# Performance work log

Measured on AMD Instinct MI355X. Metric: run time of the kernel, lower is better.

Reference implementation:

```python
import jax, jax.numpy as jnp
import numpy as np

N = 8192          # num nodes
F = 256           # feature_size
D = 128           # graph_embedding_size
E = 262144        # num edges (avg degree 32)
SLOPE = 0.2       # cfg.negativeslope
NEG_INF = -9e15   # matches torch's -9000000000000000.0 mask value


def setup_inputs() -> dict:
    key = jax.random.key(0)
    k1, k2, k3, k4 = jax.random.split(key, 4)
    X = jax.random.normal(k1, (N, F), dtype=jnp.float32)
    edge_index = jax.random.randint(k2, (2, E), 0, N, dtype=jnp.int64)
    # glorot init for Ws, xavier_uniform(gain=1.414) for a
    lim_ws = np.sqrt(6.0 / (F + D)).astype(np.float32)
    Ws = jax.random.uniform(k3, (F, D), jnp.float32, -lim_ws, lim_ws)
    lim_a = (1.414 * np.sqrt(6.0 / (2 * D + 1))).astype(np.float32)
    a = jax.random.uniform(k4, (2 * D, 1), jnp.float32, -lim_a, lim_a)
    return {"edge_index": edge_index, "X": X, "Ws": Ws, "a": a}


def reference(edge_index, X, Ws, a):
    # dense adjacency mask from edge list (sparse_coo_tensor(...).to_dense())
    adj = jnp.zeros((N, N), jnp.float32).at[edge_index[0], edge_index[1]].set(1.0)
    Wh = X @ Ws                                   # [N, D]
    # GAT-style score: Wh1_i + Wh2_j, then leaky relu
    e = jax.nn.leaky_relu(Wh @ a[:D] + (Wh @ a[D:]).T, SLOPE)  # [N, N]
    scores = jnp.where(adj > 0, e, NEG_INF)
    att = jax.nn.softmax(scores, axis=1)          # masked row softmax
    return jax.nn.elu(att @ Wh)                   # [N, D]
```

## Files before the change

### kernel.cpp

```cpp
#include <hip/hip_runtime.h>
#include <math.h>

#define N_NODES 8192
#define FDIM 256
#define DDIM 128
#define SLOPE 0.2f
#define ELLW 128

typedef __attribute__((ext_vector_type(8))) short bf16x8;
typedef __attribute__((ext_vector_type(4))) float f32x4;

__device__ __forceinline__ unsigned short f2bf(float f) {
    unsigned u = __float_as_uint(f);
    u += 0x7fffu + ((u >> 16) & 1u);
    return (unsigned short)(u >> 16);
}
__device__ __forceinline__ float bf2f(unsigned short h) {
    return __uint_as_float(((unsigned)h) << 16);
}

__global__ __launch_bounds__(256) void prep_k(const float* __restrict__ Ws,
                                              unsigned short* __restrict__ Wthi,
                                              unsigned short* __restrict__ Wtlo,
                                              unsigned* __restrict__ cnt) {
    int b = blockIdx.x, t = threadIdx.x;
    cnt[b * 256 + t] = 0u;
    if (b >= 8) return;
    __shared__ float ls[32][129];
    int k0 = b * 32;
#pragma unroll
    for (int i = 0; i < 16; i++) {
        int lin = t + 256 * i;
        int kk = lin >> 7, col = lin & 127;
        ls[kk][col] = Ws[(size_t)(k0 + kk) * DDIM + col];
    }
    __syncthreads();
    int col = t >> 1, part = t & 1;
#pragma unroll
    for (int g = 0; g < 4; g++) {
        ushort4 h, l;
        float v0 = ls[part * 16 + g * 4 + 0][col];
        float v1 = ls[part * 16 + g * 4 + 1][col];
        float v2 = ls[part * 16 + g * 4 + 2][col];
        float v3 = ls[part * 16 + g * 4 + 3][col];
        h.x = f2bf(v0); l.x = f2bf(v0 - bf2f(h.x));
        h.y = f2bf(v1); l.y = f2bf(v1 - bf2f(h.y));
        h.z = f2bf(v2); l.z = f2bf(v2 - bf2f(h.z));
        h.w = f2bf(v3); l.w = f2bf(v3 - bf2f(h.w));
        size_t o = (size_t)col * FDIM + k0 + part * 16 + g * 4;
        *(ushort4*)(Wthi + o) = h;
        *(ushort4*)(Wtlo + o) = l;
    }
}

__global__ __launch_bounds__(256) void build_ell(const int* __restrict__ edge, int E,
                                                 unsigned* __restrict__ cnt,
                                                 unsigned* __restrict__ ell) {
    int e = blockIdx.x * blockDim.x + threadIdx.x;
    if (e >= E) return;
    int r = edge[e];
    int c = edge[E + e];
    unsigned slot = atomicAdd(&cnt[r], 1u);
    if (slot < ELLW) ell[(size_t)r * ELLW + slot] = (unsigned)c;
}

__global__ __launch_bounds__(256) void gemm_mfma2(const float* __restrict__ X,
                                                  const unsigned short* __restrict__ Wthi,
                                                  const unsigned short* __restrict__ Wtlo,
                                                  const float* __restrict__ a,
                                                  unsigned short* __restrict__ WhB,
                                                  float* __restrict__ s1,
                                                  float* __restrict__ s2) {
    __shared__ unsigned short Ah[16 * 264], Al[16 * 264];
    __shared__ unsigned short Bh[128 * 72], Bl[128 * 72];
    __shared__ float ps1[64], ps2[64];
    int t = threadIdx.x;
    int w = t >> 6, lane = t & 63, lr = lane & 15, kg = lane >> 4;
    int row0 = blockIdx.x * 16;
    int colbase = w * 32;

    const float4* Xg = (const float4*)(X + (size_t)row0 * FDIM);
#pragma unroll
    for (int i = 0; i < 4; i++) {
        int lin = t + 256 * i;
        int r = lin >> 6, q = lin & 63;
        float4 v = Xg[r * 64 + q];
        ushort4 h, l;
        h.x = f2bf(v.x); l.x = f2bf(v.x - bf2f(h.x));
        h.y = f2bf(v.y); l.y = f2bf(v.y - bf2f(h.y));
        h.z = f2bf(v.z); l.z = f2bf(v.z - bf2f(h.z));
        h.w = f2bf(v.w); l.w = f2bf(v.w - bf2f(h.w));
        *(ushort4*)(Ah + r * 264 + q * 4) = h;
        *(ushort4*)(Al + r * 264 + q * 4) = l;
    }

    f32x4 acc0 = (f32x4){0.f, 0.f, 0.f, 0.f};
    f32x4 acc1 = (f32x4){0.f, 0.f, 0.f, 0.f};

    for (int c = 0; c < 4; c++) {
        if (c) __syncthreads();
#pragma unroll
        for (int i = 0; i < 4; i++) {
            int lin = t + 256 * i;
            int col = lin >> 3, q = lin & 7;
            size_t src = (size_t)col * FDIM + c * 64 + q * 8;
            *(uint4*)(Bh + col * 72 + q * 8) = *(const uint4*)(Wthi + src);
            *(uint4*)(Bl + col * 72 + q * 8) = *(const uint4*)(Wtlo + src);
        }
        __syncthreads();
#pragma unroll
        for (int ks = 0; ks < 2; ks++) {
            int ko = c * 64 + ks * 32;
            bf16x8 ahi = *(bf16x8*)(Ah + lr * 264 + ko + kg * 8);
            bf16x8 alo = *(bf16x8*)(Al + lr * 264 + ko + kg * 8);
            int c0 = colbase + lr, c1 = colbase + 16 + lr;
            bf16x8 bh0 = *(bf16x8*)(Bh + c0 * 72 + ks * 32 + kg * 8);
            bf16x8 bl0 = *(bf16x8*)(Bl + c0 * 72 + ks * 32 + kg * 8);
            bf16x8 bh1 = *(bf16x8*)(Bh + c1 * 72 + ks * 32 + kg * 8);
            bf16x8 bl1 = *(bf16x8*)(Bl + c1 * 72 + ks * 32 + kg * 8);
            acc0 = __builtin_amdgcn_mfma_f32_16x16x32_bf16(ahi, bh0, acc0, 0, 0, 0);
            acc0 = __builtin_amdgcn_mfma_f32_16x16x32_bf16(ahi, bl0, acc0, 0, 0, 0);
            acc0 = __builtin_amdgcn_mfma_f32_16x16x32_bf16(alo, bh0, acc0, 0, 0, 0);
            acc1 = __builtin_amdgcn_mfma_f32_16x16x32_bf16(ahi, bh1, acc1, 0, 0, 0);
            acc1 = __builtin_amdgcn_mfma_f32_16x16x32_bf16(ahi, bl1, acc1, 0, 0, 0);
            acc1 = __builtin_amdgcn_mfma_f32_16x16x32_bf16(alo, bh1, acc1, 0, 0, 0);
        }
    }

#pragma unroll
    for (int r = 0; r < 4; r++) {
        int row = row0 + kg * 4 + r;
        int c0 = colbase + lr, c1 = colbase + 16 + lr;
        float v0 = acc0[r], v1 = acc1[r];
        WhB[(size_t)row * DDIM + c0] = f2bf(v0);
        WhB[(size_t)row * DDIM + c1] = f2bf(v1);
        float q1 = v0 * a[c0] + v1 * a[c1];
        float q2 = v0 * a[DDIM + c0] + v1 * a[DDIM + c1];
        for (int o = 1; o < 16; o <<= 1) {
            q1 += __shfl_xor(q1, o, 16);
            q2 += __shfl_xor(q2, o, 16);
        }
        if (lr == 0) { ps1[w * 16 + kg * 4 + r] = q1; ps2[w * 16 + kg * 4 + r] = q2; }
    }
    __syncthreads();
    if (t < 16) {
        s1[row0 + t] = (ps1[t] + ps1[16 + t]) + (ps1[32 + t] + ps1[48 + t]);
        s2[row0 + t] = (ps2[t] + ps2[16 + t]) + (ps2[32 + t] + ps2[48 + t]);
    }
}

__global__ __launch_bounds__(256) void row_wave_k(const unsigned* __restrict__ cnt,
                                                  const unsigned* __restrict__ ell,
                                                  const float* __restrict__ s1v,
                                                  const float* __restrict__ s2v,
                                                  const unsigned short* __restrict__ WhB,
                                                  float* __restrict__ out) {
    __shared__ unsigned bmw[4][256];
    __shared__ float    pl[4][ELLW];
    __shared__ unsigned jl[4][ELLW];

    int w = threadIdx.x >> 6, lane = threadIdx.x & 63;
    int i = blockIdx.x * 4 + w;
    const ushort2* WhB2 = (const ushort2*)WhB;

    ((uint4*)bmw[w])[lane] = make_uint4(0u, 0u, 0u, 0u);
    unsigned deg = cnt[i];
    if (deg > ELLW) deg = ELLW;
    __syncthreads();

    if (deg == 0u) {
        float sx = 0.f, sy = 0.f;
        for (int rr = 0; rr < N_NODES; rr++) {
            ushort2 u = WhB2[(size_t)rr * 64 + lane];
            sx += bf2f(u.x); sy += bf2f(u.y);
        }
        sx *= (1.0f / N_NODES); sy *= (1.0f / N_NODES);
        sx = sx > 0.f ? sx : __expf(sx) - 1.f;
        sy = sy > 0.f ? sy : __expf(sy) - 1.f;
        ((float2*)out)[(size_t)i * 64 + lane] = make_float2(sx, sy);
        return;
    }

    const unsigned* erow = ell + (size_t)i * ELLW;
    unsigned j0 = 0u, j1 = 0u;
    bool v0 = false, v1 = false;
    if (lane < (int)deg) j0 = erow[lane];
    if (lane + 64 < (int)deg) j1 = erow[lane + 64];
    if (lane < (int)deg) {
        unsigned m = 1u << (j0 & 31);
        v0 = !(atomicOr(&bmw[w][j0 >> 5], m) & m);
    }
    if (lane + 64 < (int)deg) {
        unsigned m = 1u << (j1 & 31);
        v1 = !(atomicOr(&bmw[w][j1 >> 5], m) & m);
    }

    float s1 = s1v[i];
    float e0 = -3e38f, e1 = -3e38f;
    if (v0) { float e = s1 + s2v[j0]; e0 = e > 0.f ? e : SLOPE * e; }
    if (v1) { float e = s1 + s2v[j1]; e1 = e > 0.f ? e : SLOPE * e; }

    float mx = fmaxf(e0, e1);
    for (int o = 32; o; o >>= 1) mx = fmaxf(mx, __shfl_xor(mx, o, 64));

    float p0 = v0 ? __expf(e0 - mx) : 0.f;
    float p1 = v1 ? __expf(e1 - mx) : 0.f;
    float s = p0 + p1;
    for (int o = 32; o; o >>= 1) s += __shfl_xor(s, o, 64);
    float inv = 1.0f / s;

    pl[w][lane] = p0;      jl[w][lane] = j0;
    pl[w][lane + 64] = p1; jl[w][lane + 64] = j1;

    float ax = 0.f, ay = 0.f;
#pragma unroll 8
    for (unsigned n = 0; n < deg; ++n) {
        float p = pl[w][n];
        unsigned j = jl[w][n];
        ushort2 u = WhB2[(size_t)j * 64 + lane];
        ax = fmaf(p, bf2f(u.x), ax);
        ay = fmaf(p, bf2f(u.y), ay);
    }
    ax *= inv; ay *= inv;
    ax = ax > 0.f ? ax : __expf(ax) - 1.f;
    ay = ay > 0.f ? ay : __expf(ay) - 1.f;
    ((float2*)out)[(size_t)i * 64 + lane] = make_float2(ax, ay);
}

extern "C" void kernel_launch(void* const* d_in, const int* in_sizes, int n_in,
                              void* d_out, int out_size, void* d_ws, size_t ws_size,
                              hipStream_t stream) {
    const int*   edge = (const int*)d_in[0];
    const float* X    = (const float*)d_in[1];
    const float* Ws   = (const float*)d_in[2];
    const float* a    = (const float*)d_in[3];
    float*       out  = (float*)d_out;
    int E = in_sizes[0] / 2;

    char* ws = (char*)d_ws;
    size_t off = 0;
    unsigned*       cnt  = (unsigned*)(ws + off); off += 32 * 1024;
    unsigned*       ell  = (unsigned*)(ws + off); off += (size_t)N_NODES * ELLW * 4;
    float*          s1   = (float*)(ws + off);    off += N_NODES * 4;
    float*          s2   = (float*)(ws + off);    off += N_NODES * 4;
    unsigned short* WhB  = (unsigned short*)(ws + off); off += (size_t)N_NODES * DDIM * 2;
    unsigned short* Wthi = (unsigned short*)(ws + off); off += (size_t)FDIM * DDIM * 2;
    unsigned short* Wtlo = (unsigned short*)(ws + off); off += (size_t)FDIM * DDIM * 2;

    prep_k<<<32, 256, 0, stream>>>(Ws, Wthi, Wtlo, cnt);
    build_ell<<<(E + 255) / 256, 256, 0, stream>>>(edge, E, cnt, ell);
    gemm_mfma2<<<N_NODES / 16, 256, 0, stream>>>(X, Wthi, Wtlo, a, WhB, s1, s2);
    row_wave_k<<<N_NODES / 4, 256, 0, stream>>>(cnt, ell, s1, s2, WhB, out);
}
```

Baseline: 40.73 us.

## Fuse ELL build and GEMM into one launch and pad degree counters

```diff
diff --git a/kernel.cpp b/kernel.cpp
--- a/kernel.cpp
+++ b/kernel.cpp
@@ -6,6 +6,7 @@
 #define DDIM 128
 #define SLOPE 0.2f
 #define ELLW 128
+#define CSTR 16
 
 typedef __attribute__((ext_vector_type(8))) short bf16x8;
 typedef __attribute__((ext_vector_type(4))) float f32x4;
@@ -24,7 +25,9 @@
                                               unsigned short* __restrict__ Wtlo,
                                               unsigned* __restrict__ cnt) {
     int b = blockIdx.x, t = threadIdx.x;
-    cnt[b * 256 + t] = 0u;
+    int zi = b * 256 + t;
+    ((uint4*)cnt)[zi] = make_uint4(0u, 0u, 0u, 0u);
+    ((uint4*)cnt)[65536 / 4 + zi] = make_uint4(0u, 0u, 0u, 0u);
     if (b >= 8) return;
     __shared__ float ls[32][129];
     int k0 = b * 32;
@@ -53,30 +56,35 @@
     }
 }
 
-__global__ __launch_bounds__(256) void build_ell(const int* __restrict__ edge, int E,
-                                                 unsigned* __restrict__ cnt,
-                                                 unsigned* __restrict__ ell) {
-    int e = blockIdx.x * blockDim.x + threadIdx.x;
-    if (e >= E) return;
-    int r = edge[e];
-    int c = edge[E + e];
-    unsigned slot = atomicAdd(&cnt[r], 1u);
-    if (slot < ELLW) ell[(size_t)r * ELLW + slot] = (unsigned)c;
-}
-
-__global__ __launch_bounds__(256) void gemm_mfma2(const float* __restrict__ X,
-                                                  const unsigned short* __restrict__ Wthi,
-                                                  const unsigned short* __restrict__ Wtlo,
-                                                  const float* __restrict__ a,
-                                                  unsigned short* __restrict__ WhB,
-                                                  float* __restrict__ s1,
-                                                  float* __restrict__ s2) {
+__global__ __launch_bounds__(256) void mega_k(const int* __restrict__ edge, int E,
+                                              const float* __restrict__ X,
+                                              const unsigned short* __restrict__ Wthi,
+                                              const unsigned short* __restrict__ Wtlo,
+                                              const float* __restrict__ a,
+                                              unsigned short* __restrict__ WhB,
+                                              float* __restrict__ s1,
+                                              float* __restrict__ s2,
+                                              unsigned* __restrict__ cnt,
+                                              unsigned* __restrict__ ell) {
+    int bid = blockIdx.x, t = threadIdx.x;
+
+    if (bid % 3) {
+        int bi = (bid / 3) * 2 + (bid % 3 - 1);
+        int e = bi * 256 + t;
+        if (e < E) {
+            int r = edge[e];
+            int c = edge[E + e];
+            unsigned slot = atomicAdd(&cnt[(size_t)r * CSTR], 1u);
+            if (slot < ELLW) ell[(size_t)r * ELLW + slot] = (unsigned)c;
+        }
+        return;
+    }
+
     __shared__ unsigned short Ah[16 * 264], Al[16 * 264];
     __shared__ unsigned short Bh[128 * 72], Bl[128 * 72];
     __shared__ float ps1[64], ps2[64];
-    int t = threadIdx.x;
     int w = t >> 6, lane = t & 63, lr = lane & 15, kg = lane >> 4;
-    int row0 = blockIdx.x * 16;
+    int row0 = (bid / 3) * 16;
     int colbase = w * 32;
 
     const float4* Xg = (const float4*)(X + (size_t)row0 * FDIM);
@@ -164,7 +172,7 @@
     const ushort2* WhB2 = (const ushort2*)WhB;
 
     ((uint4*)bmw[w])[lane] = make_uint4(0u, 0u, 0u, 0u);
-    unsigned deg = cnt[i];
+    unsigned deg = cnt[(size_t)i * CSTR];
     if (deg > ELLW) deg = ELLW;
     __syncthreads();
 
@@ -239,7 +247,7 @@
 
     char* ws = (char*)d_ws;
     size_t off = 0;
-    unsigned*       cnt  = (unsigned*)(ws + off); off += 32 * 1024;
+    unsigned*       cnt  = (unsigned*)(ws + off); off += (size_t)N_NODES * CSTR * 4;
     unsigned*       ell  = (unsigned*)(ws + off); off += (size_t)N_NODES * ELLW * 4;
     float*          s1   = (float*)(ws + off);    off += N_NODES * 4;
     float*          s2   = (float*)(ws + off);    off += N_NODES * 4;
@@ -247,8 +255,7 @@
     unsigned short* Wthi = (unsigned short*)(ws + off); off += (size_t)FDIM * DDIM * 2;
     unsigned short* Wtlo = (unsigned short*)(ws + off); off += (size_t)FDIM * DDIM * 2;
 
-    prep_k<<<32, 256, 0, stream>>>(Ws, Wthi, Wtlo, cnt);
-    build_ell<<<(E + 255) / 256, 256, 0, stream>>>(edge, E, cnt, ell);
-    gemm_mfma2<<<N_NODES / 16, 256, 0, stream>>>(X, Wthi, Wtlo, a, WhB, s1, s2);
+    prep_k<<<256, 256, 0, stream>>>(Ws, Wthi, Wtlo, cnt);
+    mega_k<<<1536, 256, 0, stream>>>(edge, E, X, Wthi, Wtlo, a, WhB, s1, s2, cnt, ell);
     row_wave_k<<<N_NODES / 4, 256, 0, stream>>>(cnt, ell, s1, s2, WhB, out);
 }
```

After: 36.17 us. 1.13x faster.
